# Kernel optimization log

Hardware: AMD Instinct MI355X
Metric: run time of the kernel (lower is better)

Reference implementation:

```python
import jax, jax.numpy as jnp
import numpy as np

B_SZ, L, H, D, N, R, K = 2, 1024, 2048, 4096, 16, 128, 4


def setup_inputs() -> dict:
    key = jax.random.key(0)
    ks = jax.random.split(key, 10)
    s = lambda *sh: 1.0 / np.sqrt(sh[-1])
    inp = {
        "hidden_states": jax.random.normal(ks[0], (B_SZ, L, H), jnp.float32),
        "in_proj_w": jax.random.normal(ks[1], (2 * D, H), jnp.float32) * s(H),
        "conv_w": jax.random.normal(ks[2], (D, 1, K), jnp.float32) * s(K),
        "conv_b": jax.random.normal(ks[3], (D,), jnp.float32) * 0.02,
        "x_proj_w": jax.random.normal(ks[4], (R + 2 * N, D), jnp.float32) * s(D),
        "dt_proj_w": jax.random.normal(ks[5], (D, R), jnp.float32) * s(R),
        "dt_proj_b": jax.random.normal(ks[6], (D,), jnp.float32) * 0.02,
        # A_log = log(arange(1, N+1)) broadcast over D, as in the module init
        "A_log": jnp.broadcast_to(jnp.log(jnp.arange(1, N + 1, dtype=jnp.float32))[None, :], (D, N)),
        "D_param": jnp.ones((D,), jnp.float32),
        "out_proj_w": jax.random.normal(ks[7], (H, D), jnp.float32) * s(D),
    }
    return inp


def _mamba_forward(hidden_states, in_proj_w, conv_w, conv_b, x_proj_w,
                   dt_proj_w, dt_proj_b, A_log, D_param, out_proj_w):
    silu = jax.nn.silu
    # in_proj: [B,L,H] @ [H,2D] -> [B,L,2D] -> [B,2D,L]
    proj = jnp.einsum("blh,ph->bpl", hidden_states, in_proj_w)
    u, gate = jnp.split(proj, 2, axis=1)  # each [B,D,L]
    # depthwise causal conv1d (padding K-1 on the left, then first L outputs)
    u = jax.lax.conv_general_dilated(
        u, conv_w, window_strides=(1,), padding=[(K - 1, 0)],
        dimension_numbers=("NCH", "OIH", "NCH"), feature_group_count=D,
    ) + conv_b[None, :, None]
    u = silu(u)  # [B,D,L]
    # x_proj on [B,L,D]
    ssm_params = jnp.einsum("bdl,pd->blp", u, x_proj_w)  # [B,L,R+2N]
    time_step, Bmat, Cmat = jnp.split(ssm_params, [R, R + N], axis=-1)
    # dt_proj + softplus -> [B,D,L]
    dt = jnp.einsum("blr,dr->bld", time_step, dt_proj_w) + dt_proj_b
    dt = jax.nn.softplus(dt).transpose(0, 2, 1)  # [B,D,L]
    A = -jnp.exp(A_log)  # [D,N]

    # selective scan over time; carry ssm_state [B,D,N]
    def step(state, xs):
        dt_t, B_t, C_t, u_t = xs  # [B,D],[B,N],[B,N],[B,D]
        dA = jnp.exp(A[None] * dt_t[:, :, None])          # [B,D,N]
        dBu = dt_t[:, :, None] * B_t[:, None, :] * u_t[:, :, None]
        state = dA * state + dBu
        y_t = jnp.einsum("bdn,bn->bd", state, C_t)        # [B,D]
        return state, y_t

    xs = (dt.transpose(2, 0, 1),          # [L,B,D]
          Bmat.transpose(1, 0, 2),        # [L,B,N]
          Cmat.transpose(1, 0, 2),        # [L,B,N]
          u.transpose(2, 0, 1))           # [L,B,D]
    init = jnp.zeros((hidden_states.shape[0], D, N), hidden_states.dtype)
    _, ys = jax.lax.scan(step, init, xs)   # ys [L,B,D]
    y = ys.transpose(1, 2, 0)              # [B,D,L]
    y = y + u * D_param[None, :, None]
    y = y * silu(gate)
    # out_proj: [B,L,D] @ [D,H]
    return jnp.einsum("bdl,hd->blh", y, out_proj_w)


def reference(hidden_states, in_proj_w, conv_w, conv_b, x_proj_w,
              dt_proj_w, dt_proj_b, A_log, D_param, out_proj_w):
    return _mamba_forward(hidden_states, in_proj_w, conv_w, conv_b, x_proj_w,
                          dt_proj_w, dt_proj_b, A_log, D_param, out_proj_w)
```

## Files before the change

kernel.cpp:

```cpp
#include <hip/hip_runtime.h>

#define L_SEQ 1024
#define DD 4096
#define NC 16
#define CT 64

typedef short bf16x8 __attribute__((ext_vector_type(8)));
typedef float f32x4 __attribute__((ext_vector_type(4)));
typedef unsigned short u16;

typedef const __attribute__((address_space(1))) void gas_t;
typedef __attribute__((address_space(3))) void las_t;

__device__ inline u16 f2bf(float f) {
  unsigned int u = __float_as_uint(f);
  u = (u + 0x7FFFu + ((u >> 16) & 1u)) >> 16;
  return (u16)u;
}

__device__ inline float bf2f(u16 v) {
  return __uint_as_float(((unsigned int)v) << 16);
}

__device__ inline float softplusf(float x) {
  return x > 20.f ? x : log1pf(expf(x));
}

__global__ __launch_bounds__(256) void cast_all_k(
    const float* __restrict__ hs, const float* __restrict__ w_in,
    const float* __restrict__ xw, const float* __restrict__ dtw,
    const float* __restrict__ ow, u16* __restrict__ hs_bf,
    u16* __restrict__ win_bf, u16* __restrict__ xw_bf,
    u16* __restrict__ dtw_bf, u16* __restrict__ ow_bf) {
  const int blk = blockIdx.x;
  const float* s;
  u16* d;
  int base;
  if (blk < 4096)        { s = hs;   d = hs_bf;  base = blk; }
  else if (blk < 20480)  { s = w_in; d = win_bf; base = blk - 4096; }
  else if (blk < 21120)  { s = xw;   d = xw_bf;  base = blk - 20480; }
  else if (blk < 21632)  { s = dtw;  d = dtw_bf; base = blk - 21120; }
  else                   { s = ow;   d = ow_bf;  base = blk - 21632; }
  const int i = (base * 256 + threadIdx.x) * 4;
  float4 v = *(const float4*)(s + i);
  ushort4 o;
  o.x = f2bf(v.x); o.y = f2bf(v.y); o.z = f2bf(v.z); o.w = f2bf(v.w);
  *(ushort4*)(d + i) = o;
}

__global__ __launch_bounds__(256) void reduce4_k(const float* __restrict__ p,
                                                 float* __restrict__ out,
                                                 long n) {
  long i = ((long)blockIdx.x * 256 + threadIdx.x) * 4;
  if (i >= n) return;
  float4 a = *(const float4*)(p + i);
  float4 b = *(const float4*)(p + n + i);
  float4 c = *(const float4*)(p + 2 * n + i);
  float4 d = *(const float4*)(p + 3 * n + i);
  float4 o;
  o.x = (a.x + b.x) + (c.x + d.x);
  o.y = (a.y + b.y) + (c.y + d.y);
  o.z = (a.z + b.z) + (c.z + d.z);
  o.w = (a.w + b.w) + (c.w + d.w);
  *(float4*)(out + i) = o;
}

__global__ __launch_bounds__(256) void xproj_fin_k(const float* __restrict__ parts,
                                                   u16* __restrict__ ts,
                                                   float* __restrict__ ssm) {
  const int idx = blockIdx.x * 256 + threadIdx.x;
  float s = 0.f;
#pragma unroll
  for (int z = 0; z < 8; z++) s += parts[z * 327680 + idx];
  const int row = idx / 160;
  const int col = idx - row * 160;
  if (col < 128) ts[row * 128 + col] = f2bf(s);
  else ssm[idx] = s;
}

template <int CMODE, bool SWZ>
__global__ __launch_bounds__(512, 2) void gemm256(const u16* __restrict__ A,
                                                  const u16* __restrict__ B,
                                                  void* __restrict__ Cv,
                                                  int Nld, int K, int kc,
                                                  long zstride) {
  __shared__ u16 lds[2][2][8192];
  const int tid = threadIdx.x;
  const int lane = tid & 63, wid = tid >> 6;
  const int wm = wid >> 2, wn = wid & 3;
  int ty = blockIdx.y, tx = blockIdx.x;
  if (SWZ) {
    int flat = blockIdx.y * 32 + blockIdx.x;
    int xcd = flat & 7, pos = flat >> 3;
    ty = (xcd & 1) * 4 + (pos >> 3);
    tx = (xcd >> 1) * 8 + (pos & 7);
  }
  const long tm = (long)ty * 256, tn = (long)tx * 256;

  const long ks0 = (CMODE == 2) ? (long)blockIdx.z * kc : 0;

  const int srow = tid >> 2;
  const int sks = (((tid & 3) ^ ((srow >> 1) & 3))) * 8;
  const u16* gA0 = A + (tm + srow) * (long)K + ks0 + sks;
  const u16* gA1 = A + (tm + 128 + srow) * (long)K + ks0 + sks;
  const u16* gB0 = B + (tn + srow) * (long)K + ks0 + sks;
  const u16* gB1 = B + (tn + 128 + srow) * (long)K + ks0 + sks;
  const int sb0 = wid * 512;
  const int sb1 = 4096 + wid * 512;

  f32x4 acc[8][4] = {};

  const int lr = lane & 15, kq = lane >> 4;
  const int arow = wm * 128 + lr;
  const int brow = wn * 64 + lr;
  const int granA = (kq ^ ((arow >> 1) & 3)) * 8;
  const int granB = (kq ^ ((brow >> 1) & 3)) * 8;

  const int KT = kc >> 5;
  int cur = 0;
  __builtin_amdgcn_global_load_lds((gas_t*)gA0, (las_t*)&lds[0][0][sb0], 16, 0, 0);
  __builtin_amdgcn_global_load_lds((gas_t*)gA1, (las_t*)&lds[0][0][sb1], 16, 0, 0);
  __builtin_amdgcn_global_load_lds((gas_t*)gB0, (las_t*)&lds[0][1][sb0], 16, 0, 0);
  __builtin_amdgcn_global_load_lds((gas_t*)gB1, (las_t*)&lds[0][1][sb1], 16, 0, 0);
  __syncthreads();

  for (int kt = 0; kt < KT; ++kt) {
    if (kt + 1 < KT) {
      const long ko = (long)(kt + 1) << 5;
      const int nb = cur ^ 1;
      __builtin_amdgcn_global_load_lds((gas_t*)(gA0 + ko), (las_t*)&lds[nb][0][sb0], 16, 0, 0);
      __builtin_amdgcn_global_load_lds((gas_t*)(gA1 + ko), (las_t*)&lds[nb][0][sb1], 16, 0, 0);
      __builtin_amdgcn_global_load_lds((gas_t*)(gB0 + ko), (las_t*)&lds[nb][1][sb0], 16, 0, 0);
      __builtin_amdgcn_global_load_lds((gas_t*)(gB1 + ko), (las_t*)&lds[nb][1][sb1], 16, 0, 0);
    }
    bf16x8 af[8], bfr[4];
#pragma unroll
    for (int n = 0; n < 4; n++)
      bfr[n] = *(const bf16x8*)&lds[cur][1][(brow + n * 16) * 32 + granB];
#pragma unroll
    for (int m = 0; m < 8; m++)
      af[m] = *(const bf16x8*)&lds[cur][0][(arow + m * 16) * 32 + granA];
#pragma unroll
    for (int m = 0; m < 8; m++)
#pragma unroll
      for (int n = 0; n < 4; n++)
        acc[m][n] = __builtin_amdgcn_mfma_f32_16x16x32_bf16(af[m], bfr[n],
                                                            acc[m][n], 0, 0, 0);
    __syncthreads();
    cur ^= 1;
  }

  float* Cf = (CMODE == 2) ? (float*)Cv + (long)blockIdx.z * zstride
                           : (float*)Cv;

  const int rg = (lane >> 4) * 4;
#pragma unroll
  for (int m = 0; m < 8; m++) {
    const long gr = tm + wm * 128 + m * 16 + rg;
#pragma unroll
    for (int n = 0; n < 4; n++) {
      const long gc = tn + wn * 64 + n * 16 + lr;
#pragma unroll
      for (int r = 0; r < 4; r++) {
        if (CMODE == 1)
          ((u16*)Cv)[(gr + r) * (long)Nld + gc] = f2bf(acc[m][n][r]);
        else
          Cf[(gr + r) * (long)Nld + gc] = acc[m][n][r];
      }
    }
  }
}

template <bool CLAMP_N, int MODE>
__global__ __launch_bounds__(256) void gemm_bt(const u16* __restrict__ A,
                                               const u16* __restrict__ B,
                                               void* __restrict__ Cv,
                                               const float* __restrict__ ebias,
                                               int Nv, int K, int ldc, int kc,
                                               long zs) {
  __shared__ u16 lA[128 * 32];
  __shared__ u16 lB[128 * 32];
  const int tid = threadIdx.x;
  const int lane = tid & 63, wid = tid >> 6;
  const int wm = wid >> 1, wn = wid & 1;
  const long tm = (long)blockIdx.y * 128, tn = (long)blockIdx.x * 128;

  f32x4 acc[4][4] = {};

  const int roff = lane >> 2;
  const int sks = (((lane & 3) ^ ((roff >> 1) & 3))) * 8;
  const int c0 = wid * 2, c1 = c0 + 1;
  const long ra0 = tm + c0 * 16 + roff;
  const long ra1 = tm + c1 * 16 + roff;
  long rb0 = tn + c0 * 16 + roff;
  long rb1 = tn + c1 * 16 + roff;
  if (CLAMP_N) {
    if (rb0 >= Nv) rb0 = Nv - 1;
    if (rb1 >= Nv) rb1 = Nv - 1;
  }
  const u16* gA0 = A + ra0 * K + sks;
  const u16* gA1 = A + ra1 * K + sks;
  const u16* gB0 = B + rb0 * K + sks;
  const u16* gB1 = B + rb1 * K + sks;
  u16* sA0 = &lA[c0 * 512];
  u16* sA1 = &lA[c1 * 512];
  u16* sB0 = &lB[c0 * 512];
  u16* sB1 = &lB[c1 * 512];

  int ks0 = 0, ks1 = K;
  if (MODE == 2) { ks0 = blockIdx.z * kc; ks1 = ks0 + kc; }

  const int lr = lane & 15, kq = lane >> 4;
  const int arow = wm * 64 + lr, brow = wn * 64 + lr;
  const int granA = (kq ^ ((arow >> 1) & 3)) * 8;
  const int granB = (kq ^ ((brow >> 1) & 3)) * 8;

  for (int ks = ks0; ks < ks1; ks += 32) {
    __builtin_amdgcn_global_load_lds((gas_t*)(gA0 + ks), (las_t*)sA0, 16, 0, 0);
    __builtin_amdgcn_global_load_lds((gas_t*)(gA1 + ks), (las_t*)sA1, 16, 0, 0);
    __builtin_amdgcn_global_load_lds((gas_t*)(gB0 + ks), (las_t*)sB0, 16, 0, 0);
    __builtin_amdgcn_global_load_lds((gas_t*)(gB1 + ks), (las_t*)sB1, 16, 0, 0);
    __syncthreads();
    bf16x8 af[4], bfr[4];
#pragma unroll
    for (int i = 0; i < 4; i++) {
      af[i]  = *(const bf16x8*)&lA[(arow + i * 16) * 32 + granA];
      bfr[i] = *(const bf16x8*)&lB[(brow + i * 16) * 32 + granB];
    }
#pragma unroll
    for (int i = 0; i < 4; i++)
#pragma unroll
      for (int j = 0; j < 4; j++)
        acc[i][j] = __builtin_amdgcn_mfma_f32_16x16x32_bf16(af[i], bfr[j],
                                                            acc[i][j], 0, 0, 0);
    __syncthreads();
  }

  float* Cf = (MODE == 2) ? (float*)Cv + (long)blockIdx.z * zs : (float*)Cv;

  const int rg = (lane >> 4) * 4;
#pragma unroll
  for (int i = 0; i < 4; i++) {
    const long gr = tm + wm * 64 + i * 16 + rg;
#pragma unroll
    for (int j = 0; j < 4; j++) {
      const long gc = tn + wn * 64 + j * 16 + lr;
      if (CLAMP_N && gc >= Nv) continue;
      float bias = 0.f;
      if (MODE == 1) bias = ebias[gc];
#pragma unroll
      for (int r = 0; r < 4; r++) {
        float v = acc[i][j][r];
        if (MODE == 1)
          ((u16*)Cv)[(gr + r) * (long)ldc + gc] = f2bf(softplusf(v + bias));
        else
          Cf[(gr + r) * (long)ldc + gc] = v;
      }
    }
  }
}

__global__ __launch_bounds__(256) void conv_silu_k(const u16* __restrict__ projb,
                                                   const float* __restrict__ cw,
                                                   const float* __restrict__ cb,
                                                   u16* __restrict__ ub) {
  const int idx = blockIdx.x * 256 + threadIdx.x;
  const int d = idx & (DD - 1);
  const int bl = idx >> 12;
  const int l = bl & (L_SEQ - 1);
  const float4 w = *(const float4*)(cw + d * 4);
  float s = cb[d];
  const u16* pp = projb + (long)bl * 8192 + d;
  s += w.w * bf2f(pp[0]);
  if (l >= 1) s += w.z * bf2f(pp[-8192]);
  if (l >= 2) s += w.y * bf2f(pp[-2 * 8192]);
  if (l >= 3) s += w.x * bf2f(pp[-3 * 8192]);
  const float r = s / (1.f + expf(-s));
  ub[idx] = f2bf(r);
}

__global__ __launch_bounds__(256) void scan_p1(const u16* __restrict__ dt,
                                               const u16* __restrict__ u,
                                               const float* __restrict__ ssm,
                                               const float* __restrict__ A_log,
                                               float* __restrict__ Sbuf,
                                               float* __restrict__ Pbuf) {
  __shared__ float sBC[CT * 32];
  const int tid = threadIdx.x;
  const int d = blockIdx.x * 256 + tid;
  const int c = blockIdx.y, b = blockIdx.z;
  const long blbase = (long)b * L_SEQ + (long)c * CT;
  for (int i = tid; i < CT * 32; i += 256) {
    int tt = i >> 5, j = i & 31;
    sBC[i] = ssm[(blbase + tt) * 160 + 128 + j];
  }
  __syncthreads();
  float a2[16], st[16], pr[16];
#pragma unroll
  for (int g = 0; g < 4; g++) {
    float4 al = *(const float4*)(A_log + d * 16 + g * 4);
    a2[g*4+0] = -expf(al.x) * 1.4426950408889634f;
    a2[g*4+1] = -expf(al.y) * 1.4426950408889634f;
    a2[g*4+2] = -expf(al.z) * 1.4426950408889634f;
    a2[g*4+3] = -expf(al.w) * 1.4426950408889634f;
  }
#pragma unroll
  for (int n = 0; n < 16; n++) { st[n] = 0.f; pr[n] = 1.f; }
  for (int tt = 0; tt < CT; tt++) {
    const long bl = blbase + tt;
    const float dtv = bf2f(dt[bl * DD + d]);
    const float uv = bf2f(u[bl * DD + d]);
    const float dtu = dtv * uv;
    const float4* Bv = (const float4*)&sBC[tt * 32];
#pragma unroll
    for (int g = 0; g < 4; g++) {
      const float4 Bg = Bv[g];
      float e;
      e = exp2f(a2[g*4+0]*dtv); st[g*4+0] = e*st[g*4+0] + dtu*Bg.x; pr[g*4+0] *= e;
      e = exp2f(a2[g*4+1]*dtv); st[g*4+1] = e*st[g*4+1] + dtu*Bg.y; pr[g*4+1] *= e;
      e = exp2f(a2[g*4+2]*dtv); st[g*4+2] = e*st[g*4+2] + dtu*Bg.z; pr[g*4+2] *= e;
      e = exp2f(a2[g*4+3]*dtv); st[g*4+3] = e*st[g*4+3] + dtu*Bg.w; pr[g*4+3] *= e;
    }
  }
  const long base = (((long)b * NC + c) * DD + d) * 16;
#pragma unroll
  for (int g = 0; g < 4; g++) {
    *(float4*)(Sbuf + base + g * 4) = make_float4(st[g*4+0], st[g*4+1], st[g*4+2], st[g*4+3]);
    *(float4*)(Pbuf + base + g * 4) = make_float4(pr[g*4+0], pr[g*4+1], pr[g*4+2], pr[g*4+3]);
  }
}

__global__ __launch_bounds__(256) void scan_p2(const float* __restrict__ Sbuf,
                                               const float* __restrict__ Pbuf,
                                               float* __restrict__ carry) {
  const int idx = blockIdx.x * 256 + threadIdx.x;
  const int ng = idx & 3;
  const int d = (idx >> 2) & (DD - 1);
  const int b = idx >> 14;
  float4 cr = make_float4(0.f, 0.f, 0.f, 0.f);
  for (int c = 0; c < NC; c++) {
    const long base = (((long)b * NC + c) * DD + d) * 16 + ng * 4;
    *(float4*)(carry + base) = cr;
    const float4 P = *(const float4*)(Pbuf + base);
    const float4 S = *(const float4*)(Sbuf + base);
    cr.x = P.x * cr.x + S.x;
    cr.y = P.y * cr.y + S.y;
    cr.z = P.z * cr.z + S.z;
    cr.w = P.w * cr.w + S.w;
  }
}

__global__ __launch_bounds__(256) void scan_p3(const u16* __restrict__ dt,
                                               const u16* __restrict__ u,
                                               const float* __restrict__ ssm,
                                               const u16* __restrict__ projb,
                                               const float* __restrict__ A_log,
                                               const float* __restrict__ Dp,
                                               const float* __restrict__ carry,
                                               u16* __restrict__ yb) {
  __shared__ float sBC[CT * 32];
  const int tid = threadIdx.x;
  const int d = blockIdx.x * 256 + tid;
  const int c = blockIdx.y, b = blockIdx.z;
  const long blbase = (long)b * L_SEQ + (long)c * CT;
  for (int i = tid; i < CT * 32; i += 256) {
    int tt = i >> 5, j = i & 31;
    sBC[i] = ssm[(blbase + tt) * 160 + 128 + j];
  }
  __syncthreads();
  float a2[16], st[16];
#pragma unroll
  for (int g = 0; g < 4; g++) {
    float4 al = *(const float4*)(A_log + d * 16 + g * 4);
    a2[g*4+0] = -expf(al.x) * 1.4426950408889634f;
    a2[g*4+1] = -expf(al.y) * 1.4426950408889634f;
    a2[g*4+2] = -expf(al.z) * 1.4426950408889634f;
    a2[g*4+3] = -expf(al.w) * 1.4426950408889634f;
  }
  const long cbase = (((long)b * NC + c) * DD + d) * 16;
#pragma unroll
  for (int g = 0; g < 4; g++) {
    float4 cv = *(const float4*)(carry + cbase + g * 4);
    st[g*4+0] = cv.x; st[g*4+1] = cv.y; st[g*4+2] = cv.z; st[g*4+3] = cv.w;
  }
  const float dp = Dp[d];
  for (int tt = 0; tt < CT; tt++) {
    const long bl = blbase + tt;
    const float dtv = bf2f(dt[bl * DD + d]);
    const float uv = bf2f(u[bl * DD + d]);
    const float dtu = dtv * uv;
    float acc = 0.f;
    const float4* Bv = (const float4*)&sBC[tt * 32];
    const float4* Cv = Bv + 4;
#pragma unroll
    for (int g = 0; g < 4; g++) {
      const float4 Bg = Bv[g];
      const float4 Cg = Cv[g];
      float e;
      e = exp2f(a2[g*4+0]*dtv); st[g*4+0] = e*st[g*4+0] + dtu*Bg.x; acc += st[g*4+0]*Cg.x;
      e = exp2f(a2[g*4+1]*dtv); st[g*4+1] = e*st[g*4+1] + dtu*Bg.y; acc += st[g*4+1]*Cg.y;
      e = exp2f(a2[g*4+2]*dtv); st[g*4+2] = e*st[g*4+2] + dtu*Bg.z; acc += st[g*4+2]*Cg.z;
      e = exp2f(a2[g*4+3]*dtv); st[g*4+3] = e*st[g*4+3] + dtu*Bg.w; acc += st[g*4+3]*Cg.w;
    }
    const float g = bf2f(projb[bl * 8192 + DD + d]);
    const float yv = (acc + uv * dp) * (g / (1.f + expf(-g)));
    yb[bl * DD + d] = f2bf(yv);
  }
}

extern "C" void kernel_launch(void* const* d_in, const int* in_sizes, int n_in,
                              void* d_out, int out_size, void* d_ws, size_t ws_size,
                              hipStream_t stream) {
  const float* hs     = (const float*)d_in[0];
  const float* w_in   = (const float*)d_in[1];
  const float* conv_w = (const float*)d_in[2];
  const float* conv_b = (const float*)d_in[3];
  const float* xw     = (const float*)d_in[4];
  const float* dtw    = (const float*)d_in[5];
  const float* dtb    = (const float*)d_in[6];
  const float* A_log  = (const float*)d_in[7];
  const float* Dp     = (const float*)d_in[8];
  const float* ow     = (const float*)d_in[9];
  float* out = (float*)d_out;

  constexpr size_t SZ_HS_BF  = 2048ull * 2048 * 2;
  constexpr size_t SZ_WIN_BF = 8192ull * 2048 * 2;
  constexpr size_t SZ_PROJ   = 2048ull * 8192 * 2;
  constexpr size_t SZ_UBF    = 2048ull * 4096 * 2;
  constexpr size_t SZ_XW_BF  = 160ull * 4096 * 2;
  constexpr size_t SZ_SSM    = 2048ull * 160 * 4;
  constexpr size_t SZ_TS_BF  = 2048ull * 128 * 2;
  constexpr size_t SZ_DTW_BF = 4096ull * 128 * 2;
  constexpr size_t SZ_DT     = 2048ull * 4096 * 2;
  constexpr size_t SZ_OW_BF  = 2048ull * 4096 * 2;
  constexpr size_t SZ_YBF    = 2048ull * 4096 * 2;
  constexpr size_t SZ_SCAN   = 2ull * NC * DD * 16 * 4;
  constexpr size_t SZ_PXP    = 8ull * 2048 * 160 * 4;
  constexpr size_t TOTAL = SZ_HS_BF + SZ_WIN_BF + SZ_PROJ + SZ_UBF +
                           SZ_XW_BF + SZ_SSM + SZ_TS_BF + SZ_DTW_BF + SZ_DT +
                           SZ_OW_BF + SZ_YBF + 3 * SZ_SCAN + SZ_PXP;
  if (ws_size < TOTAL) return;

  char* w = (char*)d_ws;
  u16* hs_bf   = (u16*)w;   w += SZ_HS_BF;
  u16* win_bf  = (u16*)w;   w += SZ_WIN_BF;
  u16* projb   = (u16*)w;   w += SZ_PROJ;
  u16* u_bf    = (u16*)w;   w += SZ_UBF;
  u16* xw_bf   = (u16*)w;   w += SZ_XW_BF;
  float* ssm   = (float*)w; w += SZ_SSM;
  u16* ts_bf   = (u16*)w;   w += SZ_TS_BF;
  u16* dtw_bf  = (u16*)w;   w += SZ_DTW_BF;
  u16* dt_bf   = (u16*)w;   w += SZ_DT;
  u16* ow_bf   = (u16*)w;   w += SZ_OW_BF;
  u16* y_bf    = (u16*)w;   w += SZ_YBF;
  float* Sbuf  = (float*)w; w += SZ_SCAN;
  float* Pbuf  = (float*)w; w += SZ_SCAN;
  float* carry = (float*)w; w += SZ_SCAN;
  float* partsx = (float*)w; w += SZ_PXP;

  float* parts = (float*)win_bf;

  cast_all_k<<<29824, 256, 0, stream>>>(hs, w_in, xw, dtw, ow,
                                        hs_bf, win_bf, xw_bf, dtw_bf, ow_bf);

  gemm256<1, true><<<dim3(32, 8), 512, 0, stream>>>(
      hs_bf, win_bf, projb, 8192, 2048, 2048, 0);

  conv_silu_k<<<32768, 256, 0, stream>>>(projb, conv_w, conv_b, u_bf);

  gemm_bt<true, 2><<<dim3(2, 16, 8), 256, 0, stream>>>(
      u_bf, xw_bf, partsx, nullptr, 160, 4096, 160, 512, 327680);

  xproj_fin_k<<<1280, 256, 0, stream>>>(partsx, ts_bf, ssm);

  gemm_bt<false, 1><<<dim3(32, 16), 256, 0, stream>>>(
      ts_bf, dtw_bf, dt_bf, dtb, 4096, 128, 4096, 0, 0);

  scan_p1<<<dim3(16, NC, 2), 256, 0, stream>>>(dt_bf, u_bf, ssm, A_log, Sbuf, Pbuf);
  scan_p2<<<128, 256, 0, stream>>>(Sbuf, Pbuf, carry);
  scan_p3<<<dim3(16, NC, 2), 256, 0, stream>>>(dt_bf, u_bf, ssm, projb, A_log, Dp,
                                               carry, y_bf);

  gemm256<2, false><<<dim3(8, 8, 4), 512, 0, stream>>>(
      y_bf, ow_bf, parts, 2048, 4096, 1024, 2048ll * 2048);
  reduce4_k<<<4096, 256, 0, stream>>>(parts, out, 2048ll * 2048);
}
```

Before: 381.1 us.

## Split scan state across four threads per channel and use smaller chunks

```diff
diff --git a/kernel.cpp b/kernel.cpp
--- a/kernel.cpp
+++ b/kernel.cpp
@@ -2,8 +2,8 @@
 
 #define L_SEQ 1024
 #define DD 4096
-#define NC 16
-#define CT 64
+#define NC 32
+#define CT 32
 
 typedef short bf16x8 __attribute__((ext_vector_type(8)));
 typedef float f32x4 __attribute__((ext_vector_type(4)));
@@ -287,7 +287,8 @@
                                                float* __restrict__ Pbuf) {
   __shared__ float sBC[CT * 32];
   const int tid = threadIdx.x;
-  const int d = blockIdx.x * 256 + tid;
+  const int ng = tid & 3;
+  const int d = blockIdx.x * 64 + (tid >> 2);
   const int c = blockIdx.y, b = blockIdx.z;
   const long blbase = (long)b * L_SEQ + (long)c * CT;
   for (int i = tid; i < CT * 32; i += 256) {
@@ -295,39 +296,28 @@
     sBC[i] = ssm[(blbase + tt) * 160 + 128 + j];
   }
   __syncthreads();
-  float a2[16], st[16], pr[16];
-#pragma unroll
-  for (int g = 0; g < 4; g++) {
-    float4 al = *(const float4*)(A_log + d * 16 + g * 4);
-    a2[g*4+0] = -expf(al.x) * 1.4426950408889634f;
-    a2[g*4+1] = -expf(al.y) * 1.4426950408889634f;
-    a2[g*4+2] = -expf(al.z) * 1.4426950408889634f;
-    a2[g*4+3] = -expf(al.w) * 1.4426950408889634f;
-  }
-#pragma unroll
-  for (int n = 0; n < 16; n++) { st[n] = 0.f; pr[n] = 1.f; }
+  const float4 al = *(const float4*)(A_log + d * 16 + ng * 4);
+  const float a2x = -expf(al.x) * 1.4426950408889634f;
+  const float a2y = -expf(al.y) * 1.4426950408889634f;
+  const float a2z = -expf(al.z) * 1.4426950408889634f;
+  const float a2w = -expf(al.w) * 1.4426950408889634f;
+  float4 st = make_float4(0.f, 0.f, 0.f, 0.f);
+  float4 pr = make_float4(1.f, 1.f, 1.f, 1.f);
   for (int tt = 0; tt < CT; tt++) {
     const long bl = blbase + tt;
     const float dtv = bf2f(dt[bl * DD + d]);
     const float uv = bf2f(u[bl * DD + d]);
     const float dtu = dtv * uv;
-    const float4* Bv = (const float4*)&sBC[tt * 32];
-#pragma unroll
-    for (int g = 0; g < 4; g++) {
-      const float4 Bg = Bv[g];
-      float e;
-      e = exp2f(a2[g*4+0]*dtv); st[g*4+0] = e*st[g*4+0] + dtu*Bg.x; pr[g*4+0] *= e;
-      e = exp2f(a2[g*4+1]*dtv); st[g*4+1] = e*st[g*4+1] + dtu*Bg.y; pr[g*4+1] *= e;
-      e = exp2f(a2[g*4+2]*dtv); st[g*4+2] = e*st[g*4+2] + dtu*Bg.z; pr[g*4+2] *= e;
-      e = exp2f(a2[g*4+3]*dtv); st[g*4+3] = e*st[g*4+3] + dtu*Bg.w; pr[g*4+3] *= e;
-    }
-  }
-  const long base = (((long)b * NC + c) * DD + d) * 16;
-#pragma unroll
-  for (int g = 0; g < 4; g++) {
-    *(float4*)(Sbuf + base + g * 4) = make_float4(st[g*4+0], st[g*4+1], st[g*4+2], st[g*4+3]);
-    *(float4*)(Pbuf + base + g * 4) = make_float4(pr[g*4+0], pr[g*4+1], pr[g*4+2], pr[g*4+3]);
-  }
+    const float4 Bg = *(const float4*)&sBC[tt * 32 + ng * 4];
+    float e;
+    e = exp2f(a2x * dtv); st.x = e * st.x + dtu * Bg.x; pr.x *= e;
+    e = exp2f(a2y * dtv); st.y = e * st.y + dtu * Bg.y; pr.y *= e;
+    e = exp2f(a2z * dtv); st.z = e * st.z + dtu * Bg.z; pr.z *= e;
+    e = exp2f(a2w * dtv); st.w = e * st.w + dtu * Bg.w; pr.w *= e;
+  }
+  const long base = (((long)b * NC + c) * DD + d) * 16 + ng * 4;
+  *(float4*)(Sbuf + base) = st;
+  *(float4*)(Pbuf + base) = pr;
 }
 
 __global__ __launch_bounds__(256) void scan_p2(const float* __restrict__ Sbuf,
@@ -337,16 +327,24 @@
   const int ng = idx & 3;
   const int d = (idx >> 2) & (DD - 1);
   const int b = idx >> 14;
+  const long stride = (long)DD * 16;
+  long base = ((long)b * NC * DD + d) * 16 + ng * 4;
+  float4 P = *(const float4*)(Pbuf + base);
+  float4 S = *(const float4*)(Sbuf + base);
   float4 cr = make_float4(0.f, 0.f, 0.f, 0.f);
   for (int c = 0; c < NC; c++) {
-    const long base = (((long)b * NC + c) * DD + d) * 16 + ng * 4;
+    float4 Pn, Sn;
+    if (c + 1 < NC) {
+      Pn = *(const float4*)(Pbuf + base + stride);
+      Sn = *(const float4*)(Sbuf + base + stride);
+    }
     *(float4*)(carry + base) = cr;
-    const float4 P = *(const float4*)(Pbuf + base);
-    const float4 S = *(const float4*)(Sbuf + base);
     cr.x = P.x * cr.x + S.x;
     cr.y = P.y * cr.y + S.y;
     cr.z = P.z * cr.z + S.z;
     cr.w = P.w * cr.w + S.w;
+    P = Pn; S = Sn;
+    base += stride;
   }
 }
 
@@ -360,7 +358,8 @@
                                                u16* __restrict__ yb) {
   __shared__ float sBC[CT * 32];
   const int tid = threadIdx.x;
-  const int d = blockIdx.x * 256 + tid;
+  const int ng = tid & 3;
+  const int d = blockIdx.x * 64 + (tid >> 2);
   const int c = blockIdx.y, b = blockIdx.z;
   const long blbase = (long)b * L_SEQ + (long)c * CT;
   for (int i = tid; i < CT * 32; i += 256) {
@@ -368,43 +367,32 @@
     sBC[i] = ssm[(blbase + tt) * 160 + 128 + j];
   }
   __syncthreads();
-  float a2[16], st[16];
-#pragma unroll
-  for (int g = 0; g < 4; g++) {
-    float4 al = *(const float4*)(A_log + d * 16 + g * 4);
-    a2[g*4+0] = -expf(al.x) * 1.4426950408889634f;
-    a2[g*4+1] = -expf(al.y) * 1.4426950408889634f;
-    a2[g*4+2] = -expf(al.z) * 1.4426950408889634f;
-    a2[g*4+3] = -expf(al.w) * 1.4426950408889634f;
-  }
-  const long cbase = (((long)b * NC + c) * DD + d) * 16;
-#pragma unroll
-  for (int g = 0; g < 4; g++) {
-    float4 cv = *(const float4*)(carry + cbase + g * 4);
-    st[g*4+0] = cv.x; st[g*4+1] = cv.y; st[g*4+2] = cv.z; st[g*4+3] = cv.w;
-  }
+  const float4 al = *(const float4*)(A_log + d * 16 + ng * 4);
+  const float a2x = -expf(al.x) * 1.4426950408889634f;
+  const float a2y = -expf(al.y) * 1.4426950408889634f;
+  const float a2z = -expf(al.z) * 1.4426950408889634f;
+  const float a2w = -expf(al.w) * 1.4426950408889634f;
+  float4 st = *(const float4*)(carry + (((long)b * NC + c) * DD + d) * 16 + ng * 4);
   const float dp = Dp[d];
   for (int tt = 0; tt < CT; tt++) {
     const long bl = blbase + tt;
     const float dtv = bf2f(dt[bl * DD + d]);
     const float uv = bf2f(u[bl * DD + d]);
     const float dtu = dtv * uv;
-    float acc = 0.f;
-    const float4* Bv = (const float4*)&sBC[tt * 32];
-    const float4* Cv = Bv + 4;
-#pragma unroll
-    for (int g = 0; g < 4; g++) {
-      const float4 Bg = Bv[g];
-      const float4 Cg = Cv[g];
-      float e;
-      e = exp2f(a2[g*4+0]*dtv); st[g*4+0] = e*st[g*4+0] + dtu*Bg.x; acc += st[g*4+0]*Cg.x;
-      e = exp2f(a2[g*4+1]*dtv); st[g*4+1] = e*st[g*4+1] + dtu*Bg.y; acc += st[g*4+1]*Cg.y;
-      e = exp2f(a2[g*4+2]*dtv); st[g*4+2] = e*st[g*4+2] + dtu*Bg.z; acc += st[g*4+2]*Cg.z;
-      e = exp2f(a2[g*4+3]*dtv); st[g*4+3] = e*st[g*4+3] + dtu*Bg.w; acc += st[g*4+3]*Cg.w;
-    }
-    const float g = bf2f(projb[bl * 8192 + DD + d]);
-    const float yv = (acc + uv * dp) * (g / (1.f + expf(-g)));
-    yb[bl * DD + d] = f2bf(yv);
+    const float4 Bg = *(const float4*)&sBC[tt * 32 + ng * 4];
+    const float4 Cg = *(const float4*)&sBC[tt * 32 + 16 + ng * 4];
+    float e, acc;
+    e = exp2f(a2x * dtv); st.x = e * st.x + dtu * Bg.x; acc  = st.x * Cg.x;
+    e = exp2f(a2y * dtv); st.y = e * st.y + dtu * Bg.y; acc += st.y * Cg.y;
+    e = exp2f(a2z * dtv); st.z = e * st.z + dtu * Bg.z; acc += st.z * Cg.z;
+    e = exp2f(a2w * dtv); st.w = e * st.w + dtu * Bg.w; acc += st.w * Cg.w;
+    acc += __shfl_xor(acc, 1);
+    acc += __shfl_xor(acc, 2);
+    if (ng == 0) {
+      const float g = bf2f(projb[bl * 8192 + DD + d]);
+      const float yv = (acc + uv * dp) * (g / (1.f + expf(-g)));
+      yb[bl * DD + d] = f2bf(yv);
+    }
   }
 }
 
@@ -476,9 +464,9 @@
   gemm_bt<false, 1><<<dim3(32, 16), 256, 0, stream>>>(
       ts_bf, dtw_bf, dt_bf, dtb, 4096, 128, 4096, 0, 0);
 
-  scan_p1<<<dim3(16, NC, 2), 256, 0, stream>>>(dt_bf, u_bf, ssm, A_log, Sbuf, Pbuf);
+  scan_p1<<<dim3(64, NC, 2), 256, 0, stream>>>(dt_bf, u_bf, ssm, A_log, Sbuf, Pbuf);
   scan_p2<<<128, 256, 0, stream>>>(Sbuf, Pbuf, carry);
-  scan_p3<<<dim3(16, NC, 2), 256, 0, stream>>>(dt_bf, u_bf, ssm, projb, A_log, Dp,
+  scan_p3<<<dim3(64, NC, 2), 256, 0, stream>>>(dt_bf, u_bf, ssm, projb, A_log, Dp,
                                                carry, y_bf);
 
   gemm256<2, false><<<dim3(8, 8, 4), 512, 0, stream>>>(
```

Result: no change. 373.7 us (-1.9%).

## Halve scan chunk length, stage dt/u tiles in LDS, prefetch in scan passes

Applied to the files above, without the earlier changes.

```diff
diff --git a/kernel.cpp b/kernel.cpp
--- a/kernel.cpp
+++ b/kernel.cpp
@@ -2,8 +2,8 @@
 
 #define L_SEQ 1024
 #define DD 4096
-#define NC 16
-#define CT 64
+#define NC 32
+#define CT 32
 
 typedef short bf16x8 __attribute__((ext_vector_type(8)));
 typedef float f32x4 __attribute__((ext_vector_type(4)));
@@ -286,13 +286,25 @@
                                                float* __restrict__ Sbuf,
                                                float* __restrict__ Pbuf) {
   __shared__ float sBC[CT * 32];
+  __shared__ u16 dtl[CT][256];
+  __shared__ u16 ul[CT][256];
   const int tid = threadIdx.x;
-  const int d = blockIdx.x * 256 + tid;
+  const int d0 = blockIdx.x * 256;
+  const int d = d0 + tid;
   const int c = blockIdx.y, b = blockIdx.z;
   const long blbase = (long)b * L_SEQ + (long)c * CT;
   for (int i = tid; i < CT * 32; i += 256) {
     int tt = i >> 5, j = i & 31;
     sBC[i] = ssm[(blbase + tt) * 160 + 128 + j];
+  }
+  const u16* dtg = dt + blbase * DD + d0;
+  const u16* ug  = u  + blbase * DD + d0;
+#pragma unroll
+  for (int it = 0; it < 4; ++it) {
+    const int ck = it * 256 + tid;
+    const int row = ck >> 5, ch = (ck & 31) * 8;
+    *(uint4*)&dtl[row][ch] = *(const uint4*)(dtg + (long)row * DD + ch);
+    *(uint4*)&ul[row][ch]  = *(const uint4*)(ug  + (long)row * DD + ch);
   }
   __syncthreads();
   float a2[16], st[16], pr[16];
@@ -307,9 +319,8 @@
 #pragma unroll
   for (int n = 0; n < 16; n++) { st[n] = 0.f; pr[n] = 1.f; }
   for (int tt = 0; tt < CT; tt++) {
-    const long bl = blbase + tt;
-    const float dtv = bf2f(dt[bl * DD + d]);
-    const float uv = bf2f(u[bl * DD + d]);
+    const float dtv = bf2f(dtl[tt][tid]);
+    const float uv = bf2f(ul[tt][tid]);
     const float dtu = dtv * uv;
     const float4* Bv = (const float4*)&sBC[tt * 32];
 #pragma unroll
@@ -337,16 +348,24 @@
   const int ng = idx & 3;
   const int d = (idx >> 2) & (DD - 1);
   const int b = idx >> 14;
+  const long stride = (long)DD * 16;
+  long base = ((long)b * NC * DD + d) * 16 + ng * 4;
+  float4 P = *(const float4*)(Pbuf + base);
+  float4 S = *(const float4*)(Sbuf + base);
   float4 cr = make_float4(0.f, 0.f, 0.f, 0.f);
   for (int c = 0; c < NC; c++) {
-    const long base = (((long)b * NC + c) * DD + d) * 16 + ng * 4;
+    float4 Pn, Sn;
+    if (c + 1 < NC) {
+      Pn = *(const float4*)(Pbuf + base + stride);
+      Sn = *(const float4*)(Sbuf + base + stride);
+    }
     *(float4*)(carry + base) = cr;
-    const float4 P = *(const float4*)(Pbuf + base);
-    const float4 S = *(const float4*)(Sbuf + base);
     cr.x = P.x * cr.x + S.x;
     cr.y = P.y * cr.y + S.y;
     cr.z = P.z * cr.z + S.z;
     cr.w = P.w * cr.w + S.w;
+    P = Pn; S = Sn;
+    base += stride;
   }
 }
 
@@ -359,13 +378,25 @@
                                                const float* __restrict__ carry,
                                                u16* __restrict__ yb) {
   __shared__ float sBC[CT * 32];
+  __shared__ u16 dtl[CT][256];
+  __shared__ u16 ul[CT][256];
   const int tid = threadIdx.x;
-  const int d = blockIdx.x * 256 + tid;
+  const int d0 = blockIdx.x * 256;
+  const int d = d0 + tid;
   const int c = blockIdx.y, b = blockIdx.z;
   const long blbase = (long)b * L_SEQ + (long)c * CT;
   for (int i = tid; i < CT * 32; i += 256) {
     int tt = i >> 5, j = i & 31;
     sBC[i] = ssm[(blbase + tt) * 160 + 128 + j];
+  }
+  const u16* dtg = dt + blbase * DD + d0;
+  const u16* ug  = u  + blbase * DD + d0;
+#pragma unroll
+  for (int it = 0; it < 4; ++it) {
+    const int ck = it * 256 + tid;
+    const int row = ck >> 5, ch = (ck & 31) * 8;
+    *(uint4*)&dtl[row][ch] = *(const uint4*)(dtg + (long)row * DD + ch);
+    *(uint4*)&ul[row][ch]  = *(const uint4*)(ug  + (long)row * DD + ch);
   }
   __syncthreads();
   float a2[16], st[16];
@@ -384,10 +415,13 @@
     st[g*4+0] = cv.x; st[g*4+1] = cv.y; st[g*4+2] = cv.z; st[g*4+3] = cv.w;
   }
   const float dp = Dp[d];
+  const u16* gp = projb + blbase * 8192 + DD + d;
+  u16 gnext = gp[0];
   for (int tt = 0; tt < CT; tt++) {
-    const long bl = blbase + tt;
-    const float dtv = bf2f(dt[bl * DD + d]);
-    const float uv = bf2f(u[bl * DD + d]);
+    const u16 gcur = gnext;
+    if (tt + 1 < CT) gnext = gp[(tt + 1) * 8192];
+    const float dtv = bf2f(dtl[tt][tid]);
+    const float uv = bf2f(ul[tt][tid]);
     const float dtu = dtv * uv;
     float acc = 0.f;
     const float4* Bv = (const float4*)&sBC[tt * 32];
@@ -402,9 +436,9 @@
       e = exp2f(a2[g*4+2]*dtv); st[g*4+2] = e*st[g*4+2] + dtu*Bg.z; acc += st[g*4+2]*Cg.z;
       e = exp2f(a2[g*4+3]*dtv); st[g*4+3] = e*st[g*4+3] + dtu*Bg.w; acc += st[g*4+3]*Cg.w;
     }
-    const float g = bf2f(projb[bl * 8192 + DD + d]);
+    const float g = bf2f(gcur);
     const float yv = (acc + uv * dp) * (g / (1.f + expf(-g)));
-    yb[bl * DD + d] = f2bf(yv);
+    yb[(blbase + tt) * DD + d] = f2bf(yv);
   }
 }
 
```

After: 355.4 us. -6.7%, faster.
